# Performance work log

Measured on AMD Instinct MI355X. Metric: run time of the kernel, lower is better.

The kernel has to match this reference:

```python
import jax, jax.numpy as jnp
import numpy as np

# Multi-scale feature pyramid (H, W) per level, standard Deformable-DETR for ~800x800 input
SHAPES = [(100, 100), (50, 50), (25, 25), (13, 13)]
D = 256      # d_model
NH = 8       # n_heads
NL = 4       # n_levels
NP = 4       # n_points
HD = D // NH # head_dim = 32
B = 2
S = sum(h * w for h, w in SHAPES)  # 13294
Lq = S  # encoder-style: one query per multi-scale token


def setup_inputs() -> dict:
    key = jax.random.key(0)
    ks = jax.random.split(key, 11)
    return {
        "query": jax.random.normal(ks[0], (B, Lq, D), jnp.float32),
        "reference_points": jax.random.uniform(ks[1], (B, Lq, NL, 2), jnp.float32),
        "value": jax.random.normal(ks[2], (B, S, D), jnp.float32),
        "W_val": jax.random.normal(ks[3], (D, D), jnp.float32) * 0.02,
        "b_val": jnp.zeros((D,), jnp.float32),
        "W_off": jax.random.normal(ks[4], (D, NH * NL * NP * 2), jnp.float32) * 0.01,
        "b_off": jax.random.normal(ks[5], (NH * NL * NP * 2,), jnp.float32) * 0.5,
        "W_attn": jax.random.normal(ks[6], (D, NH * NL * NP), jnp.float32) * 0.02,
        "b_attn": jnp.zeros((NH * NL * NP,), jnp.float32),
        "W_out": jax.random.normal(ks[7], (D, D), jnp.float32) * 0.02,
        "b_out": jnp.zeros((D,), jnp.float32),
    }


def _bilinear_sample(valf, x, y, H, W):
    """grid_sample(mode=bilinear, padding_mode=zeros, align_corners=False).
    valf: [N, H*W, C] flattened feature map; x, y: [N, P] pixel-space coords
    (already converted via x = loc_x*W - 0.5). Returns [N, P, C].
    """
    x0 = jnp.floor(x); y0 = jnp.floor(y)
    x1 = x0 + 1.0;     y1 = y0 + 1.0
    wx1 = x - x0; wx0 = 1.0 - wx1
    wy1 = y - y0; wy0 = 1.0 - wy1

    def corner(xi, yi, w):
        inb = (xi >= 0) & (xi <= W - 1) & (yi >= 0) & (yi <= H - 1)
        xi_c = jnp.clip(xi, 0, W - 1).astype(jnp.int32)
        yi_c = jnp.clip(yi, 0, H - 1).astype(jnp.int32)
        idx = yi_c * W + xi_c                                   # [N, P]
        v = jnp.take_along_axis(valf, idx[..., None], axis=1)   # [N, P, C]
        return v * (w * inb.astype(valf.dtype))[..., None]

    return (corner(x0, y0, wx0 * wy0) + corner(x1, y0, wx1 * wy0)
            + corner(x0, y1, wx0 * wy1) + corner(x1, y1, wx1 * wy1))


def reference(query, reference_points, value, W_val, b_val, W_off, b_off,
              W_attn, b_attn, W_out, b_out):
    Bq, L, _ = query.shape
    # value projection, split into heads: [B, S, NH, HD]
    val = (value @ W_val + b_val).reshape(Bq, S, NH, HD)
    # sampling offsets and attention weights from query
    offsets = (query @ W_off + b_off).reshape(Bq, L, NH, NL, NP, 2)
    w = (query @ W_attn + b_attn).reshape(Bq, L, NH, NL * NP)
    w = jax.nn.softmax(w, axis=-1).reshape(Bq, L, NH, NL, NP)
    # normalize offsets by (W, H) per level; 2D reference points path
    offset_norm = jnp.array([[wd, h] for h, wd in SHAPES], jnp.float32)  # [NL, 2]
    locs = (reference_points[:, :, None, :, None, :]
            + offsets / offset_norm[None, None, None, :, None, :])       # [B,L,NH,NL,NP,2]

    splits = [h * wd for h, wd in SHAPES]
    starts = np.concatenate([[0], np.cumsum(splits)])
    out_acc = jnp.zeros((Bq, L, NH, HD), query.dtype)
    for lvl, (H, W) in enumerate(SHAPES):
        vl = val[:, starts[lvl]:starts[lvl + 1]]                 # [B, HW, NH, HD]
        vl = vl.transpose(0, 2, 1, 3).reshape(Bq * NH, H * W, HD)
        loc = locs[:, :, :, lvl].transpose(0, 2, 1, 3, 4).reshape(Bq * NH, L * NP, 2)
        x = loc[..., 0] * W - 0.5   # align_corners=False pixel coords
        y = loc[..., 1] * H - 0.5
        s = _bilinear_sample(vl, x, y, H, W).reshape(Bq, NH, L, NP, HD)
        wl = w[:, :, :, lvl].transpose(0, 2, 1, 3)               # [B, NH, L, NP]
        out_acc = out_acc + jnp.einsum('bhqpd,bhqp->bqhd', s, wl)
    out = out_acc.reshape(Bq, L, NH * HD)
    return out @ W_out + b_out
```

## Files before the change

### kernel.cpp

```cpp
#include <hip/hip_runtime.h>
#include <hip/hip_bf16.h>
#include <math.h>

#define B_    2
#define NH_   8
#define NL_   4
#define NP_   4
#define HD_   32
#define S_    13294
#define L_    13294
#define M_    26588

__device__ __constant__ int c_H[NL_]     = {100, 50, 25, 13};
__device__ __constant__ int c_W[NL_]     = {100, 50, 25, 13};
__device__ __constant__ int c_start[NL_] = {0, 10000, 12500, 13125};

typedef __attribute__((ext_vector_type(8))) _Float16 f16x8;
typedef __attribute__((ext_vector_type(4))) _Float16 f16x4;
typedef __attribute__((ext_vector_type(2))) _Float16 f16x2;
typedef __attribute__((ext_vector_type(4))) float    float4v;

__device__ __forceinline__ unsigned short f2h(float f) {
    _Float16 h = (_Float16)f;
    return __builtin_bit_cast(unsigned short, h);
}
__device__ __forceinline__ float h2f(unsigned short u) {
    _Float16 h = __builtin_bit_cast(_Float16, u);
    return (float)h;
}
__device__ __forceinline__ f16x2 pkrtz(float a, float b) {
    return __builtin_bit_cast(f16x2, __builtin_amdgcn_cvt_pkrtz(a, b));
}

__global__ __launch_bounds__(256) void prep_weights(
    const float* __restrict__ W_val, const float* __restrict__ W_off,
    const float* __restrict__ W_attn, const float* __restrict__ b_off,
    const float* __restrict__ b_attn, const float* __restrict__ W_out,
    unsigned short* __restrict__ wt_val, unsigned short* __restrict__ wt_oa,
    unsigned short* __restrict__ wt_out, float* __restrict__ bias_oa)
{
    int i = blockIdx.x * 256 + threadIdx.x;
    if (i < 65536) {
        int n = i >> 8, k = i & 255;
        wt_val[i] = f2h(W_val[k * 256 + n]);
    } else if (i < 65536 + 98304) {
        int j = i - 65536;
        int n = j >> 8, k = j & 255;
        float v = (n < 256) ? W_off[k * 256 + n] : W_attn[k * 128 + (n - 256)];
        wt_oa[j] = f2h(v);
    } else if (i < 65536 + 98304 + 65536) {
        int j = i - 163840;
        int n = j >> 8, k = j & 255;
        wt_out[j] = f2h(W_out[k * 256 + n]);
    } else if (i < 229376 + 384) {
        int j = i - 229376;
        bias_oa[j] = (j < 256) ? b_off[j] : b_attn[j - 256];
    }
}

template<int N, int OUT, bool AF32>
__device__ __forceinline__ void gemm32_body(
    const void* __restrict__ Av,
    const unsigned short* __restrict__ WT,
    const float* __restrict__ bias,
    void* __restrict__ Cv,
    unsigned short (* __restrict__ As)[32][40])
{
    constexpr int NT = N / 64;

    const int tid  = threadIdx.x;
    const int lane = tid & 63;
    const int wave = tid >> 6;
    const int rowBase = blockIdx.x * 32;
    const int wcol = wave * (N / 4);

    const int r  = tid >> 3;
    const int ko = (tid & 7) * 4;
    int arow = rowBase + r; if (arow >= M_) arow = M_ - 1;

    const int fr = lane & 15;
    const int fk = (lane >> 4) * 8;

    const unsigned short* bb[NT];
#pragma unroll
    for (int t = 0; t < NT; ++t)
        bb[t] = WT + (size_t)(wcol + t * 16 + fr) * 256 + fk;

    float4 raf[4];
    f16x4  rah[4];
    f16x8 curB[NT], nxtB[NT];
    float4v acc[2][NT] = {};

    auto ldA = [&](int slot, int bk) {
        if constexpr (AF32) {
            raf[slot] = *reinterpret_cast<const float4*>(
                (const float*)Av + (size_t)arow * 256 + bk * 32 + ko);
        } else {
            rah[slot] = *reinterpret_cast<const f16x4*>(
                (const unsigned short*)Av + (size_t)arow * 256 + bk * 32 + ko);
        }
    };
    auto stA = [&](int slot, int buf) {
        f16x4 v;
        if constexpr (AF32) {
            f16x2 p0 = pkrtz(raf[slot].x, raf[slot].y);
            f16x2 p1 = pkrtz(raf[slot].z, raf[slot].w);
            v[0] = p0[0]; v[1] = p0[1]; v[2] = p1[0]; v[3] = p1[1];
        } else {
            v = rah[slot];
        }
        *reinterpret_cast<f16x4*>(&As[buf][r][ko]) = v;
    };

#pragma unroll
    for (int c = 0; c < 4; ++c) ldA(c, c);
#pragma unroll
    for (int t = 0; t < NT; ++t)
        curB[t] = *reinterpret_cast<const f16x8*>(bb[t]);
    stA(0, 0);

#pragma unroll
    for (int it = 0; it < 8; ++it) {
        __syncthreads();
        f16x8 af0 = *reinterpret_cast<const f16x8*>(&As[it & 1][fr][fk]);
        f16x8 af1 = *reinterpret_cast<const f16x8*>(&As[it & 1][16 + fr][fk]);
        if (it < 7) {
            stA((it + 1) & 3, (it + 1) & 1);
            if (it < 4) ldA(it & 3, it + 4);
#pragma unroll
            for (int t = 0; t < NT; ++t)
                nxtB[t] = *reinterpret_cast<const f16x8*>(bb[t] + (it + 1) * 32);
        }
#pragma unroll
        for (int nt = 0; nt < NT; ++nt) {
            acc[0][nt] = __builtin_amdgcn_mfma_f32_16x16x32_f16(af0, curB[nt], acc[0][nt], 0, 0, 0);
            acc[1][nt] = __builtin_amdgcn_mfma_f32_16x16x32_f16(af1, curB[nt], acc[1][nt], 0, 0, 0);
        }
        if (it < 7) {
#pragma unroll
            for (int t = 0; t < NT; ++t) curB[t] = nxtB[t];
        }
    }

    const int dn  = lane & 15;
    const int dm0 = (lane >> 4) * 4;
#pragma unroll
    for (int mt = 0; mt < 2; ++mt)
#pragma unroll
        for (int nt = 0; nt < NT; ++nt) {
            const int col = wcol + nt * 16 + dn;
            const float bv = bias[col];
#pragma unroll
            for (int rr = 0; rr < 4; ++rr) {
                const int row = rowBase + mt * 16 + dm0 + rr;
                if (row < M_) {
                    const float v = acc[mt][nt][rr] + bv;
                    if constexpr (OUT == 0)
                        ((unsigned short*)Cv)[(size_t)row * 256 + col] = f2h(v);
                    else if constexpr (OUT == 1)
                        ((unsigned short*)Cv)[(size_t)row * 384 + col] = f2h(v);
                    else
                        ((float*)Cv)[(size_t)row * 256 + col] = v;
                }
            }
        }
}

__global__ __launch_bounds__(256) void gemm_vq(
    const float* __restrict__ value, const float* __restrict__ query,
    const unsigned short* __restrict__ wt_val, const unsigned short* __restrict__ wt_oa,
    const float* __restrict__ b_val, const float* __restrict__ bias_oa,
    unsigned short* __restrict__ val_f16, unsigned short* __restrict__ oa_f16)
{
    __shared__ unsigned short As[2][32][40];
    if (blockIdx.y == 0)
        gemm32_body<256, 0, true>(value, wt_val, b_val, val_f16, As);
    else
        gemm32_body<384, 1, true>(query, wt_oa, bias_oa, oa_f16, As);
}

__global__ __launch_bounds__(256) void gemm_out4(
    const unsigned short* __restrict__ Af16,
    const unsigned short* __restrict__ WT,
    const float* __restrict__ bias, float* __restrict__ C)
{
    __shared__ unsigned short As[2][32][40];
    gemm32_body<256, 2, false>(Af16, WT, bias, C, As);
}

__global__ __launch_bounds__(256) void deform_sample_v5(
    const unsigned short* __restrict__ val,
    const float* __restrict__ refp,
    const unsigned short* __restrict__ oa,
    unsigned short* __restrict__ acc)
{
    const int tid = threadIdx.x;
    const int q0  = blockIdx.x * 8;

    __shared__ unsigned short sLog[8][128];
    __shared__ float sMS[8][8][2];
    __shared__ int   sPack[8][4][16][8];

    {
        const int q  = tid >> 5;
        const int f  = tid & 31;
        const int bq = min(q0 + q, M_ - 1);
        *reinterpret_cast<int2*>(&sLog[q][f * 4]) =
            *reinterpret_cast<const int2*>(oa + (size_t)bq * 384 + 256 + f * 4);
    }
    __syncthreads();

    if (tid < 64) {
        const int q = tid >> 3, h = tid & 7;
        float m = -1e30f;
#pragma unroll
        for (int i = 0; i < 16; ++i) m = fmaxf(m, h2f(sLog[q][h * 16 + i]));
        float s = 0.f;
#pragma unroll
        for (int i = 0; i < 16; ++i) s += __expf(h2f(sLog[q][h * 16 + i]) - m);
        sMS[q][h][0] = m;
        sMS[q][h][1] = 1.f / s;
    }
    __syncthreads();

#pragma unroll
    for (int k = 0; k < 4; ++k) {
        const int e   = tid + k * 256;
        const int q   = e >> 7;
        const int t   = e & 127;
        const int h   = t >> 4;
        const int lp  = t & 15;
        const int lvl = lp >> 2;
        const int p   = lp & 3;
        const int bq  = min(q0 + q, M_ - 1);

        const float wgt = __expf(h2f(sLog[q][t]) - sMS[q][h][0]) * sMS[q][h][1];

        const int Wi = c_W[lvl], Hi = c_H[lvl], st = c_start[lvl];
        const float rx = refp[((size_t)bq * NL_ + lvl) * 2 + 0];
        const float ry = refp[((size_t)bq * NL_ + lvl) * 2 + 1];
        const float ox = h2f(oa[(size_t)bq * 384 + h * 32 + lvl * 8 + p * 2 + 0]);
        const float oy = h2f(oa[(size_t)bq * 384 + h * 32 + lvl * 8 + p * 2 + 1]);
        const float x = rx * (float)Wi + ox - 0.5f;
        const float y = ry * (float)Hi + oy - 0.5f;

        const float x0f = floorf(x), y0f = floorf(y);
        const int   x0 = (int)x0f,   y0 = (int)y0f;
        const float wx1 = x - x0f, wx0 = 1.f - wx1;
        const float wy1 = y - y0f, wy0 = 1.f - wy1;

        const int   cx[4] = {x0, x0 + 1, x0,     x0 + 1};
        const int   cy[4] = {y0, y0,     y0 + 1, y0 + 1};
        const float cw[4] = {wx0 * wy0, wx1 * wy0, wx0 * wy1, wx1 * wy1};
#pragma unroll
        for (int c = 0; c < 4; ++c) {
            const bool inb = (cx[c] >= 0) & (cx[c] < Wi) & (cy[c] >= 0) & (cy[c] < Hi);
            const int xi = min(max(cx[c], 0), Wi - 1);
            const int yi = min(max(cy[c], 0), Hi - 1);
            const int idx = st + yi * Wi + xi;
            const unsigned short wh = f2h(inb ? wgt * cw[c] : 0.f);
            sPack[q][c][lp][h] = idx | ((int)wh << 16);
        }
    }
    __syncthreads();

    const int q  = tid >> 5;
    const int h  = (tid >> 2) & 7;
    const int d4 = tid & 3;
    const int bq = q0 + q;
    const int b  = min(bq, M_ - 1) / L_;
    const unsigned short* vb = val + (size_t)b * S_ * 256 + h * 32 + d4 * 8;

    f16x2 A0{}, A1{}, A2{}, A3{};
#pragma unroll 8
    for (int i = 0; i < 64; ++i) {
        const int lp = i >> 2;
        const int c  = i & 3;
        const int pk = sPack[q][c][lp][h];
        const unsigned wb = (unsigned)pk >> 16;
        const f16x2 w2 = __builtin_bit_cast(f16x2, (wb << 16) | wb);
        const int4 u = *reinterpret_cast<const int4*>(
            vb + (size_t)((unsigned)pk & 0xffffu) * 256);
        A0 += w2 * __builtin_bit_cast(f16x2, u.x);
        A1 += w2 * __builtin_bit_cast(f16x2, u.y);
        A2 += w2 * __builtin_bit_cast(f16x2, u.z);
        A3 += w2 * __builtin_bit_cast(f16x2, u.w);
    }
    if (bq < M_) {
        int4 o;
        o.x = __builtin_bit_cast(int, A0);
        o.y = __builtin_bit_cast(int, A1);
        o.z = __builtin_bit_cast(int, A2);
        o.w = __builtin_bit_cast(int, A3);
        *reinterpret_cast<int4*>(acc + (size_t)bq * 256 + h * 32 + d4 * 8) = o;
    }
}

extern "C" void kernel_launch(void* const* d_in, const int* in_sizes, int n_in,
                              void* d_out, int out_size, void* d_ws, size_t ws_size,
                              hipStream_t stream) {
    const float* query  = (const float*)d_in[0];
    const float* refp   = (const float*)d_in[1];
    const float* value  = (const float*)d_in[2];
    const float* W_val  = (const float*)d_in[3];
    const float* b_val  = (const float*)d_in[4];
    const float* W_off  = (const float*)d_in[5];
    const float* b_off  = (const float*)d_in[6];
    const float* W_attn = (const float*)d_in[7];
    const float* b_attn = (const float*)d_in[8];
    const float* W_out  = (const float*)d_in[9];
    const float* b_out  = (const float*)d_in[10];
    float* out = (float*)d_out;

    char* ws = (char*)d_ws;
    const size_t mb = (size_t)M_ * 256;
    unsigned short* val_f16 = (unsigned short*)ws;  ws += mb * 2;
    unsigned short* acc_f16 = (unsigned short*)ws;  ws += mb * 2;
    unsigned short* oa_f16  = (unsigned short*)ws;  ws += (size_t)M_ * 384 * 2;
    unsigned short* wt_val  = (unsigned short*)ws;  ws += 65536 * 2;
    unsigned short* wt_oa   = (unsigned short*)ws;  ws += 98304 * 2;
    unsigned short* wt_out  = (unsigned short*)ws;  ws += 65536 * 2;
    float*          bias_oa = (float*)ws;           ws += 384 * 4;

    dim3 blk(256);

    prep_weights<<<dim3(898), blk, 0, stream>>>(
        W_val, W_off, W_attn, b_off, b_attn, W_out, wt_val, wt_oa, wt_out, bias_oa);

    gemm_vq<<<dim3((M_ + 31) / 32, 2), blk, 0, stream>>>(
        value, query, wt_val, wt_oa, b_val, bias_oa, val_f16, oa_f16);

    deform_sample_v5<<<dim3((M_ + 7) / 8), blk, 0, stream>>>(val_f16, refp, oa_f16, acc_f16);

    gemm_out4<<<dim3((M_ + 31) / 32), blk, 0, stream>>>(acc_f16, wt_out, b_out, out);
}
```

Measured before the change: 226.3 us.

## Make GEMMs persistent with register-resident weight fragments across multiple row tiles

The projection GEMMs now launch a fixed grid where each block processes several 32-row tiles and loads its whole B-weight slice into registers once, instead of reloading weights per tile. The query/offset-attention GEMM is split into column groups (4+2 subtiles) to balance work across blocks, and the A-load prefetch pipeline continues across tile boundaries. This cuts redundant weight reads and launch/tail overhead, but raises register pressure (launch bounds of 2 blocks per CU) and reduces the number of blocks available to hide latency.

Result: faster. 215.8 us (-4.7%).

```diff
diff --git a/kernel.cpp b/kernel.cpp
--- a/kernel.cpp
+++ b/kernel.cpp
@@ -10,6 +10,7 @@
 #define S_    13294
 #define L_    13294
 #define M_    26588
+#define NTILE 831
 
 __device__ __constant__ int c_H[NL_]     = {100, 50, 25, 13};
 __device__ __constant__ int c_W[NL_]     = {100, 50, 25, 13};
@@ -58,47 +59,50 @@
     }
 }
 
-template<int N, int OUT, bool AF32>
-__device__ __forceinline__ void gemm32_body(
+template<int NT, int OUT, bool AF32>
+__device__ __forceinline__ void gemm_persist(
     const void* __restrict__ Av,
     const unsigned short* __restrict__ WT,
     const float* __restrict__ bias,
     void* __restrict__ Cv,
+    int t0, int t1, int colBase,
     unsigned short (* __restrict__ As)[32][40])
 {
-    constexpr int NT = N / 64;
-
     const int tid  = threadIdx.x;
     const int lane = tid & 63;
     const int wave = tid >> 6;
-    const int rowBase = blockIdx.x * 32;
-    const int wcol = wave * (N / 4);
+    const int wcol = colBase + wave * (NT * 16);
 
     const int r  = tid >> 3;
     const int ko = (tid & 7) * 4;
-    int arow = rowBase + r; if (arow >= M_) arow = M_ - 1;
-
     const int fr = lane & 15;
     const int fk = (lane >> 4) * 8;
 
-    const unsigned short* bb[NT];
-#pragma unroll
-    for (int t = 0; t < NT; ++t)
-        bb[t] = WT + (size_t)(wcol + t * 16 + fr) * 256 + fk;
-
+    f16x8 Bf[NT][8];
+#pragma unroll
+    for (int t = 0; t < NT; ++t) {
+        const unsigned short* bp = WT + (size_t)(wcol + t * 16 + fr) * 256 + fk;
+#pragma unroll
+        for (int kc = 0; kc < 8; ++kc)
+            Bf[t][kc] = *reinterpret_cast<const f16x8*>(bp + kc * 32);
+    }
+
+    const int nChunk = (t1 - t0) * 8;
     float4 raf[4];
     f16x4  rah[4];
-    f16x8 curB[NT], nxtB[NT];
-    float4v acc[2][NT] = {};
-
-    auto ldA = [&](int slot, int bk) {
-        if constexpr (AF32) {
+
+    auto ldA = [&](int slot, int g) {
+        if (g >= nChunk) g = nChunk - 1;
+        const int tile = t0 + (g >> 3);
+        int row = tile * 32 + r;
+        if (row >= M_) row = M_ - 1;
+        const int kk = (g & 7) * 32 + ko;
+        if constexpr (AF32)
             raf[slot] = *reinterpret_cast<const float4*>(
-                (const float*)Av + (size_t)arow * 256 + bk * 32 + ko);
-        } else {
+                (const float*)Av + (size_t)row * 256 + kk);
+        else
             rah[slot] = *reinterpret_cast<const f16x4*>(
-                (const unsigned short*)Av + (size_t)arow * 256 + bk * 32 + ko);
-        }
+                (const unsigned short*)Av + (size_t)row * 256 + kk);
     };
     auto stA = [&](int slot, int buf) {
         f16x4 v;
@@ -114,78 +118,81 @@
 
 #pragma unroll
     for (int c = 0; c < 4; ++c) ldA(c, c);
-#pragma unroll
-    for (int t = 0; t < NT; ++t)
-        curB[t] = *reinterpret_cast<const f16x8*>(bb[t]);
     stA(0, 0);
-
-#pragma unroll
-    for (int it = 0; it < 8; ++it) {
-        __syncthreads();
-        f16x8 af0 = *reinterpret_cast<const f16x8*>(&As[it & 1][fr][fk]);
-        f16x8 af1 = *reinterpret_cast<const f16x8*>(&As[it & 1][16 + fr][fk]);
-        if (it < 7) {
-            stA((it + 1) & 3, (it + 1) & 1);
-            if (it < 4) ldA(it & 3, it + 4);
-#pragma unroll
-            for (int t = 0; t < NT; ++t)
-                nxtB[t] = *reinterpret_cast<const f16x8*>(bb[t] + (it + 1) * 32);
-        }
-#pragma unroll
-        for (int nt = 0; nt < NT; ++nt) {
-            acc[0][nt] = __builtin_amdgcn_mfma_f32_16x16x32_f16(af0, curB[nt], acc[0][nt], 0, 0, 0);
-            acc[1][nt] = __builtin_amdgcn_mfma_f32_16x16x32_f16(af1, curB[nt], acc[1][nt], 0, 0, 0);
-        }
-        if (it < 7) {
-#pragma unroll
-            for (int t = 0; t < NT; ++t) curB[t] = nxtB[t];
-        }
-    }
 
     const int dn  = lane & 15;
     const int dm0 = (lane >> 4) * 4;
-#pragma unroll
-    for (int mt = 0; mt < 2; ++mt)
-#pragma unroll
-        for (int nt = 0; nt < NT; ++nt) {
-            const int col = wcol + nt * 16 + dn;
-            const float bv = bias[col];
-#pragma unroll
-            for (int rr = 0; rr < 4; ++rr) {
-                const int row = rowBase + mt * 16 + dm0 + rr;
-                if (row < M_) {
-                    const float v = acc[mt][nt][rr] + bv;
-                    if constexpr (OUT == 0)
-                        ((unsigned short*)Cv)[(size_t)row * 256 + col] = f2h(v);
-                    else if constexpr (OUT == 1)
-                        ((unsigned short*)Cv)[(size_t)row * 384 + col] = f2h(v);
-                    else
-                        ((float*)Cv)[(size_t)row * 256 + col] = v;
+
+    int g = 0;
+    for (int tile = t0; tile < t1; ++tile) {
+        float4v acc[2][NT] = {};
+#pragma unroll
+        for (int it = 0; it < 8; ++it) {
+            __syncthreads();
+            f16x8 af0 = *reinterpret_cast<const f16x8*>(&As[it & 1][fr][fk]);
+            f16x8 af1 = *reinterpret_cast<const f16x8*>(&As[it & 1][16 + fr][fk]);
+            if (g + 1 < nChunk) {
+                stA((g + 1) & 3, (g + 1) & 1);
+                ldA(g & 3, g + 4);
+            }
+#pragma unroll
+            for (int nt = 0; nt < NT; ++nt) {
+                acc[0][nt] = __builtin_amdgcn_mfma_f32_16x16x32_f16(af0, Bf[nt][it], acc[0][nt], 0, 0, 0);
+                acc[1][nt] = __builtin_amdgcn_mfma_f32_16x16x32_f16(af1, Bf[nt][it], acc[1][nt], 0, 0, 0);
+            }
+            ++g;
+        }
+#pragma unroll
+        for (int mt = 0; mt < 2; ++mt)
+#pragma unroll
+            for (int nt = 0; nt < NT; ++nt) {
+                const int col = wcol + nt * 16 + dn;
+                const float bv = bias[col];
+#pragma unroll
+                for (int rr = 0; rr < 4; ++rr) {
+                    const int row = tile * 32 + mt * 16 + dm0 + rr;
+                    if (row < M_) {
+                        const float v = acc[mt][nt][rr] + bv;
+                        if constexpr (OUT == 0)
+                            ((unsigned short*)Cv)[(size_t)row * 256 + col] = f2h(v);
+                        else if constexpr (OUT == 1)
+                            ((unsigned short*)Cv)[(size_t)row * 384 + col] = f2h(v);
+                        else
+                            ((float*)Cv)[(size_t)row * 256 + col] = v;
+                    }
                 }
             }
-        }
-}
-
-__global__ __launch_bounds__(256) void gemm_vq(
+    }
+}
+
+__global__ __launch_bounds__(256, 2) void gemm_vq_p(
     const float* __restrict__ value, const float* __restrict__ query,
     const unsigned short* __restrict__ wt_val, const unsigned short* __restrict__ wt_oa,
     const float* __restrict__ b_val, const float* __restrict__ bias_oa,
     unsigned short* __restrict__ val_f16, unsigned short* __restrict__ oa_f16)
 {
     __shared__ unsigned short As[2][32][40];
-    if (blockIdx.y == 0)
-        gemm32_body<256, 0, true>(value, wt_val, b_val, val_f16, As);
-    else
-        gemm32_body<384, 1, true>(query, wt_oa, bias_oa, oa_f16, As);
-}
-
-__global__ __launch_bounds__(256) void gemm_out4(
+    const int bid = blockIdx.x;
+    if (bid < 208) {
+        const int t0 = bid * 4, t1 = min(t0 + 4, NTILE);
+        gemm_persist<4, 0, true>(value, wt_val, b_val, val_f16, t0, t1, 0, As);
+    } else if (bid < 416) {
+        const int t0 = (bid - 208) * 4, t1 = min(t0 + 4, NTILE);
+        gemm_persist<4, 1, true>(query, wt_oa, bias_oa, oa_f16, t0, t1, 0, As);
+    } else {
+        const int t0 = (bid - 416) * 8, t1 = min(t0 + 8, NTILE);
+        gemm_persist<2, 1, true>(query, wt_oa, bias_oa, oa_f16, t0, t1, 256, As);
+    }
+}
+
+__global__ __launch_bounds__(256, 2) void gemm_out_p(
     const unsigned short* __restrict__ Af16,
     const unsigned short* __restrict__ WT,
     const float* __restrict__ bias, float* __restrict__ C)
 {
     __shared__ unsigned short As[2][32][40];
-    gemm32_body<256, 2, false>(Af16, WT, bias, C, As);
+    const int t0 = blockIdx.x * 2, t1 = min(t0 + 2, NTILE);
+    gemm_persist<4, 2, false>(Af16, WT, bias, C, t0, t1, 0, As);
 }
 
 __global__ __launch_bounds__(256) void deform_sample_v5(
@@ -327,10 +334,10 @@
     prep_weights<<<dim3(898), blk, 0, stream>>>(
         W_val, W_off, W_attn, b_off, b_attn, W_out, wt_val, wt_oa, wt_out, bias_oa);
 
-    gemm_vq<<<dim3((M_ + 31) / 32, 2), blk, 0, stream>>>(
+    gemm_vq_p<<<dim3(520), blk, 0, stream>>>(
         value, query, wt_val, wt_oa, b_val, bias_oa, val_f16, oa_f16);
 
     deform_sample_v5<<<dim3((M_ + 7) / 8), blk, 0, stream>>>(val_f16, refp, oa_f16, acc_f16);
 
-    gemm_out4<<<dim3((M_ + 31) / 32), blk, 0, stream>>>(acc_f16, wt_out, b_out, out);
-}
+    gemm_out_p<<<dim3(416), blk, 0, stream>>>(acc_f16, wt_out, b_out, out);
+}
```
